# Performance work log

Measured on AMD Instinct MI355X. Metric: run time of the kernel, lower is better.

The kernel has to match this reference:

```python
import jax, jax.numpy as jnp
import numpy as np
import math

EMB = 64
NEG_INF = -1e30

def _layernorm(x, g, b, eps=1e-5):
    mu = jnp.mean(x, axis=-1, keepdims=True)
    var = jnp.mean((x - mu) ** 2, axis=-1, keepdims=True)
    return (x - mu) * jax.lax.rsqrt(var + eps) * g + b

def setup_inputs() -> dict:
    key = jax.random.key(0)
    ks = jax.random.split(key, 8)
    b, t, n, d = 16, 12, 307, EMB
    s = 1.0 / math.sqrt(d)
    inp = {
        'x': jax.random.normal(ks[0], (b, t, n, d), dtype=jnp.float32),
        'stg': jax.random.uniform(ks[1], (b, n, t, n), dtype=jnp.float32),
        'topk': 3,
        'q_w': jax.random.normal(ks[2], (d, d), dtype=jnp.float32) * s,
        'q_b': jnp.zeros((d,), jnp.float32),
        'k_w': jax.random.normal(ks[3], (d, d), dtype=jnp.float32) * s,
        'k_b': jnp.zeros((d,), jnp.float32),
        'ln_g': jnp.ones((d,), jnp.float32),
        'ln_b': jnp.zeros((d,), jnp.float32),
        'ffn_ln_g': jnp.ones((d,), jnp.float32),
        'ffn_ln_b': jnp.zeros((d,), jnp.float32),
        'fc1_w': jax.random.normal(ks[4], (4 * d, d), dtype=jnp.float32) * s,
        'fc1_b': jnp.zeros((4 * d,), jnp.float32),
        'fc2_w': jax.random.normal(ks[5], (d, 4 * d), dtype=jnp.float32) * (0.5 * s),
        'fc2_b': jnp.zeros((d,), jnp.float32),
    }
    return inp

def reference(x, stg, topk, q_w, q_b, k_w, k_b, ln_g, ln_b, ffn_ln_g, ffn_ln_b, fc1_w, fc1_b, fc2_w, fc2_b):
    b, t, n, d = x.shape
    scale = 1.0 / math.sqrt(d)
    x_ = _layernorm(x, ln_g, ln_b)           # [b,t,n,d]
    y_ = x_[:, -1]                            # [b,n,d] last timestep
    q = y_ @ q_w.T + q_b                      # [b,n,d]
    k = x_ @ k_w.T + k_b                      # [b,t,n,d]
    dg = jnp.einsum('bnd,btmd->bntm', q, k) * scale
    sag = jax.nn.sigmoid(dg) * stg * scale    # gated scores [b,n,t,n]
    sag = sag.reshape(b, n, t * n)
    if topk > 0:
        kk = topk * n if topk < 5 else topk   # mirrors torch's self.topk *= n
        top_values, _ = jax.lax.top_k(sag, kk)
        thr = top_values[..., -1:]
        sag = jnp.where(sag > thr, sag, NEG_INF)  # strict >, as in torch code
    sag = jax.nn.softmax(sag, axis=-1).reshape(b, n, t, n)  # dropout in eval mode = identity
    o = jnp.einsum('bntm,btmd->bnd', sag, x_)
    h = o + y_
    # FFN: pre-norm residual MLP (LayerNorm -> Linear(d,4d) -> ReLU -> Linear(4d,d) + residual)
    z = _layernorm(h, ffn_ln_g, ffn_ln_b)
    z = jax.nn.relu(z @ fc1_w.T + fc1_b) @ fc2_w.T + fc2_b
    return h + z
```

## Files before the change

### kernel.cpp

```cpp
#include <hip/hip_runtime.h>

typedef __bf16 bf16x8 __attribute__((ext_vector_type(8)));
typedef float  f32x4  __attribute__((ext_vector_type(4)));
typedef unsigned short u16x8 __attribute__((ext_vector_type(8)));

constexpr int BB    = 16;
constexpr int TT    = 12;
constexpr int NN    = 307;
constexpr int TN    = TT * NN;
constexpr int ROWSX = BB * TT * NN;
constexpr int ROWSH = BB * NN;
constexpr int SST1  = 3712;
constexpr int SSTR  = 3840;
constexpr float SCALE = 0.125f;

__device__ __forceinline__ float wred_sum(float v) {
#pragma unroll
    for (int m = 32; m > 0; m >>= 1) v += __shfl_xor(v, m, 64);
    return v;
}

__global__ void fold_k(const float* __restrict__ qw, const float* __restrict__ qb,
                       const float* __restrict__ kw, const float* __restrict__ kb,
                       float* __restrict__ M, float* __restrict__ b2,
                       float* __restrict__ vv, float* __restrict__ cc) {
    int e = blockIdx.x, d = threadIdx.x;
    float acc = 0.f;
    for (int dp = 0; dp < 64; ++dp) acc += qw[dp * 64 + e] * kw[dp * 64 + d];
    M[e * 64 + d] = acc;
    float vp = wred_sum(qw[d * 64 + e] * kb[d]);
    if (d == 0) vv[e] = vp;
    if (e == 0) {
        float b = 0.f;
        for (int dp = 0; dp < 64; ++dp) b += qb[dp] * kw[dp * 64 + d];
        b2[d] = b;
        float cp = wred_sum(qb[d] * kb[d]);
        if (d == 0) *cc = cp;
    }
}

__global__ void wconv_k(const float* __restrict__ fc1w, const float* __restrict__ fc2w,
                        __bf16* __restrict__ fc1b16, __bf16* __restrict__ fc2b16) {
    int i = blockIdx.x * 256 + threadIdx.x;
    if (i < 16384) fc1b16[i] = (__bf16)fc1w[i];
    else fc2b16[i - 16384] = (__bf16)fc2w[i - 16384];
}

__global__ __launch_bounds__(256) void ln_k(const float* __restrict__ x,
                                            const float* __restrict__ g,
                                            const float* __restrict__ b,
                                            __bf16* __restrict__ xnb,
                                            float* __restrict__ y32) {
    int w = threadIdx.x >> 6, l = threadIdx.x & 63;
    int r = blockIdx.x * 4 + w;
    if (r >= ROWSX) return;
    float val = x[r * 64 + l];
    float mu  = wred_sum(val) * (1.f / 64.f);
    float dv  = val - mu;
    float var = wred_sum(dv * dv) * (1.f / 64.f);
    float xv  = dv * rsqrtf(var + 1e-5f) * g[l] + b[l];
    xnb[(size_t)r * 64 + l] = (__bf16)xv;
    int t = (r / NN) % TT;
    if (t == TT - 1) {
        int bbv = r / (NN * TT), n = r % NN;
        y32[(bbv * NN + n) * 64 + l] = xv;
    }
}

__global__ __launch_bounds__(256) void t_k(const __bf16* __restrict__ xnb,
                                           __bf16* __restrict__ xnT) {
    __shared__ unsigned short tile[64][65];
    int bb = blockIdx.y, j0 = blockIdx.x * 64, t = threadIdx.x;
    const unsigned short* src = (const unsigned short*)xnb;
    unsigned short* dst = (unsigned short*)xnT;
#pragma unroll
    for (int i = 0; i < 16; ++i) {
        int f = t + 256 * i, jr = f >> 6, dc = f & 63;
        int j = j0 + jr;
        tile[jr][dc] = (j < TN) ? src[((size_t)bb * TN + j) * 64 + dc] : (unsigned short)0;
    }
    __syncthreads();
#pragma unroll
    for (int i = 0; i < 16; ++i) {
        int f = t + 256 * i, d = f >> 6, jj = f & 63;
        dst[((size_t)bb * 64 + d) * SSTR + j0 + jj] = tile[jj][d];
    }
}

__global__ __launch_bounds__(256) void qt_k(const float* __restrict__ y32,
                                            const float* __restrict__ M,
                                            const float* __restrict__ b2,
                                            const float* __restrict__ vv,
                                            const float* __restrict__ ccp,
                                            __bf16* __restrict__ qtb,
                                            float* __restrict__ cq) {
    int w = threadIdx.x >> 6, l = threadIdx.x & 63;
    int rr = blockIdx.x * 4 + w;
    if (rr >= ROWSH) return;
    float y = y32[rr * 64 + l];
    float acc = b2[l];
#pragma unroll
    for (int e = 0; e < 64; ++e) acc += __shfl(y, e, 64) * M[e * 64 + l];
    qtb[(size_t)rr * 64 + l] = (__bf16)acc;
    float cp = wred_sum(y * vv[l]);
    if (l == 0) cq[rr] = cp + *ccp;
}

__global__ __launch_bounds__(256) void score_k(const __bf16* __restrict__ qtb,
                                               const float* __restrict__ cq,
                                               const __bf16* __restrict__ xnb,
                                               const float* __restrict__ stg,
                                               __bf16* __restrict__ sag) {
    __shared__ float sstg[64 * 132];
    int bb = blockIdx.z, n0 = blockIdx.y * 64, j0 = blockIdx.x * 128;
    int t = threadIdx.x;
    int w = t >> 6, lane = t & 63;
    int m16 = lane & 15, q4 = lane >> 4;

#pragma unroll
    for (int i = 0; i < 8; ++i) {
        int flat = t + i * 256;
        int row = flat >> 5, c4 = (flat & 31) * 4;
        int n = n0 + row;
        float4 v = {0.f, 0.f, 0.f, 0.f};
        if (n < NN) {
            size_t rb = (size_t)(bb * NN + n) * TN;
            int j = j0 + c4;
            if (j + 3 < TN) v = *(const float4*)(stg + rb + j);
            else {
                if (j + 0 < TN) v.x = stg[rb + j + 0];
                if (j + 1 < TN) v.y = stg[rb + j + 1];
                if (j + 2 < TN) v.z = stg[rb + j + 2];
                if (j + 3 < TN) v.w = stg[rb + j + 3];
            }
        }
        *(float4*)&sstg[row * 132 + c4] = v;
    }

    const bf16x8* ap = (const bf16x8*)(qtb + ((size_t)bb * NN + n0 + w * 16 + m16) * 64);
    bf16x8 a0 = ap[q4], a1 = ap[q4 + 4];
    f32x4 acc[8];
#pragma unroll
    for (int jt = 0; jt < 8; ++jt) {
        const bf16x8* bp = (const bf16x8*)(xnb + ((size_t)bb * TN + j0 + jt * 16 + m16) * 64);
        bf16x8 b0 = bp[q4], b1 = bp[q4 + 4];
        f32x4 c = {0.f, 0.f, 0.f, 0.f};
        c = __builtin_amdgcn_mfma_f32_16x16x32_bf16(a0, b0, c, 0, 0, 0);
        c = __builtin_amdgcn_mfma_f32_16x16x32_bf16(a1, b1, c, 0, 0, 0);
        acc[jt] = c;
    }
    int nbase = n0 + w * 16 + q4 * 4;
    float cn[4];
#pragma unroll
    for (int r = 0; r < 4; ++r) {
        int n = nbase + r;
        cn[r] = (n < NN) ? cq[bb * NN + n] : 0.f;
    }
    __syncthreads();

    u16x8 wvr[4];
#pragma unroll
    for (int r = 0; r < 4; ++r) {
        int nloc = w * 16 + q4 * 4 + r;
#pragma unroll
        for (int jt = 0; jt < 8; ++jt) {
            int j = j0 + jt * 16 + m16;
            float sv = sstg[nloc * 132 + jt * 16 + m16];
            float dg = (acc[jt][r] + cn[r]) * SCALE;
            float s  = 1.f / (1.f + __expf(-dg));
            float wv = (j < TN) ? s * sv * SCALE : 0.f;
            __bf16 wb16 = (__bf16)wv;
            wvr[r][jt] = *(unsigned short*)&wb16;
        }
    }
    __syncthreads();

    unsigned short* wb = (unsigned short*)sstg;
#pragma unroll
    for (int r = 0; r < 4; ++r) {
        int nloc = w * 16 + q4 * 4 + r;
#pragma unroll
        for (int jt = 0; jt < 8; ++jt)
            wb[nloc * 136 + jt * 16 + m16] = wvr[r][jt];
    }
    __syncthreads();

#pragma unroll
    for (int i = 0; i < 4; ++i) {
        int chunk = t + i * 256;
        int row = chunk >> 4, c8 = (chunk & 15) * 8;
        int n = n0 + row;
        if (n < NN) {
            u16x8 v = *(const u16x8*)&wb[row * 136 + c8];
            *(u16x8*)((unsigned short*)sag + (size_t)(bb * NN + n) * SST1 + j0 + c8) = v;
        }
    }
}

__global__ __launch_bounds__(256) void smax_k(__bf16* __restrict__ sagB,
                                              const int* __restrict__ topk_p) {
    int t = threadIdx.x;
    int wid = t >> 6, lane = t & 63;
    int row = blockIdx.x * 4 + wid;
    if (row >= ROWSH) return;

    int topkv = *topk_p;
    bool selAll = (topkv <= 0);
    int kk = 0;
    if (!selAll) {
        kk = (topkv < 5) ? topkv * NN : topkv;
        if (kk > TN) kk = TN;
    }

    u16x8* src = (u16x8*)((unsigned short*)sagB + (size_t)row * SST1);
    u16x8 va[8];
#pragma unroll
    for (int ci = 0; ci < 8; ++ci) {
        int c = lane + (ci << 6);
        u16x8 v = {0, 0, 0, 0, 0, 0, 0, 0};
        if (c < 464) v = src[c];
        va[ci] = v;
    }
    int vmb = 0;
#pragma unroll
    for (int ci = 0; ci < 8; ++ci)
#pragma unroll
        for (int e = 0; e < 8; ++e) vmb = max(vmb, (int)va[ci][e]);
#pragma unroll
    for (int m = 32; m > 0; m >>= 1) vmb = max(vmb, __shfl_xor(vmb, m, 64));
    float vmax = __uint_as_float(((unsigned)vmb) << 16);

    unsigned thrb = 0;
    if (!selAll) {
        unsigned lo = 0, hi = (unsigned)vmb;
        while (lo < hi) {
            unsigned mid = (lo + hi) >> 1;
            int cnt = 0;
#pragma unroll
            for (int ci = 0; ci < 8; ++ci)
#pragma unroll
                for (int e = 0; e < 8; ++e)
                    cnt += (int)__popcll(__ballot((unsigned)va[ci][e] > mid));
            if (cnt < kk) hi = mid; else lo = mid + 1;
        }
        thrb = lo;
    }

    float local = 0.f;
#pragma unroll
    for (int ci = 0; ci < 8; ++ci) {
        int c = lane + (ci << 6);
        int nvv = (c < 460) ? 8 : ((c == 460) ? 4 : 0);
#pragma unroll
        for (int e = 0; e < 8; ++e) {
            unsigned u = va[ci][e];
            bool sel = selAll ? (e < nvv) : (u > thrb);
            float ev = sel ? __expf(__uint_as_float(u << 16) - vmax) : 0.f;
            local += ev;
            __bf16 eb = (__bf16)ev;
            va[ci][e] = *(unsigned short*)&eb;
        }
    }
    local = wred_sum(local);
    bool uni = !(local > 0.f);
    float inv = uni ? 0.f : 1.f / local;
    float uval = 1.f / (float)TN;
#pragma unroll
    for (int ci = 0; ci < 8; ++ci) {
        int c = lane + (ci << 6);
        if (c < 464) {
            int nvv = (c < 460) ? 8 : ((c == 460) ? 4 : 0);
            bf16x8 o;
#pragma unroll
            for (int e = 0; e < 8; ++e) {
                if (uni) o[e] = (e < nvv) ? (__bf16)uval : (__bf16)0.f;
                else {
                    unsigned short us = va[ci][e];
                    float ev = (float)(*(__bf16*)&us);
                    o[e] = (__bf16)(ev * inv);
                }
            }
            *(bf16x8*)&src[c] = o;
        }
    }
}

__global__ __launch_bounds__(256) void pv_k(const __bf16* __restrict__ sagB,
                                            const __bf16* __restrict__ xnT,
                                            const float* __restrict__ y32,
                                            float* __restrict__ h) {
    int bb = blockIdx.y, n0 = blockIdx.x * 16;
    int wid = threadIdx.x >> 6, lane = threadIdx.x & 63;
    int m16 = lane & 15, q4 = lane >> 4;

    int arow = min(n0 + m16, NN - 1);
    const __bf16* ab  = sagB + (size_t)(bb * NN + arow) * SST1 + q4 * 8;
    const __bf16* bbp = xnT + ((size_t)bb * 64 + wid * 16 + m16) * SSTR + q4 * 8;

    f32x4 acc0 = {0.f, 0.f, 0.f, 0.f}, acc1 = {0.f, 0.f, 0.f, 0.f};
#pragma unroll 4
    for (int ks = 0; ks < 116; ks += 2) {
        bf16x8 a0 = *(const bf16x8*)(ab + ks * 32);
        bf16x8 b0 = *(const bf16x8*)(bbp + ks * 32);
        bf16x8 a1 = *(const bf16x8*)(ab + ks * 32 + 32);
        bf16x8 b1 = *(const bf16x8*)(bbp + ks * 32 + 32);
        acc0 = __builtin_amdgcn_mfma_f32_16x16x32_bf16(a0, b0, acc0, 0, 0, 0);
        acc1 = __builtin_amdgcn_mfma_f32_16x16x32_bf16(a1, b1, acc1, 0, 0, 0);
    }
#pragma unroll
    for (int r = 0; r < 4; ++r) {
        int n = n0 + q4 * 4 + r;
        if (n < NN) {
            size_t o = (size_t)(bb * NN + n) * 64 + wid * 16 + m16;
            h[o] = acc0[r] + acc1[r] + y32[o];
        }
    }
}

__global__ __launch_bounds__(256) void ffn_k(const float* __restrict__ h,
                                             const float* __restrict__ g,
                                             const float* __restrict__ bln,
                                             const __bf16* __restrict__ fc1b16,
                                             const float* __restrict__ fc1b,
                                             const __bf16* __restrict__ fc2b16,
                                             const float* __restrict__ fc2b,
                                             float* __restrict__ out) {
    __shared__ __bf16 zb[16 * 68];
    __shared__ __bf16 ab[16 * 264];
    int t = threadIdx.x, r0 = blockIdx.x * 16;
    int wid = t >> 6, lane = t & 63;
    int m16 = lane & 15, q4 = lane >> 4;

#pragma unroll
    for (int q = 0; q < 4; ++q) {
        int rl = wid * 4 + q;
        float val = h[(size_t)(r0 + rl) * 64 + lane];
        float mu  = wred_sum(val) * (1.f / 64.f);
        float dv  = val - mu;
        float var = wred_sum(dv * dv) * (1.f / 64.f);
        zb[rl * 68 + lane] = (__bf16)(dv * rsqrtf(var + 1e-5f) * g[lane] + bln[lane]);
    }
    __syncthreads();

    bf16x8 a0 = *(const bf16x8*)&zb[m16 * 68 + q4 * 8];
    bf16x8 a1 = *(const bf16x8*)&zb[m16 * 68 + 32 + q4 * 8];
#pragma unroll
    for (int jt2 = 0; jt2 < 4; ++jt2) {
        int j0t = (wid * 4 + jt2) * 16;
        const __bf16* bp = fc1b16 + (size_t)(j0t + m16) * 64 + q4 * 8;
        f32x4 c = {0.f, 0.f, 0.f, 0.f};
        c = __builtin_amdgcn_mfma_f32_16x16x32_bf16(a0, *(const bf16x8*)bp, c, 0, 0, 0);
        c = __builtin_amdgcn_mfma_f32_16x16x32_bf16(a1, *(const bf16x8*)(bp + 32), c, 0, 0, 0);
        int j = j0t + m16;
        float bias = fc1b[j];
#pragma unroll
        for (int r = 0; r < 4; ++r)
            ab[(q4 * 4 + r) * 264 + j] = (__bf16)fmaxf(c[r] + bias, 0.f);
    }
    __syncthreads();

    f32x4 c2a = {0.f, 0.f, 0.f, 0.f}, c2b = {0.f, 0.f, 0.f, 0.f};
    const __bf16* b2p = fc2b16 + (size_t)(wid * 16 + m16) * 256 + q4 * 8;
#pragma unroll
    for (int k8 = 0; k8 < 8; k8 += 2) {
        bf16x8 aa0 = *(const bf16x8*)&ab[m16 * 264 + k8 * 32 + q4 * 8];
        bf16x8 aa1 = *(const bf16x8*)&ab[m16 * 264 + (k8 + 1) * 32 + q4 * 8];
        c2a = __builtin_amdgcn_mfma_f32_16x16x32_bf16(aa0, *(const bf16x8*)(b2p + k8 * 32), c2a, 0, 0, 0);
        c2b = __builtin_amdgcn_mfma_f32_16x16x32_bf16(aa1, *(const bf16x8*)(b2p + (k8 + 1) * 32), c2b, 0, 0, 0);
    }
    int d = wid * 16 + m16;
    float bias2 = fc2b[d];
#pragma unroll
    for (int r = 0; r < 4; ++r) {
        size_t row = (size_t)(r0 + q4 * 4 + r);
        out[row * 64 + d] = h[row * 64 + d] + c2a[r] + c2b[r] + bias2;
    }
}

extern "C" void kernel_launch(void* const* d_in, const int* in_sizes, int n_in,
                              void* d_out, int out_size, void* d_ws, size_t ws_size,
                              hipStream_t stream) {
    const float* x    = (const float*)d_in[0];
    const float* stg  = (const float*)d_in[1];
    const int*   topk = (const int*)d_in[2];
    const float* qw   = (const float*)d_in[3];
    const float* qb   = (const float*)d_in[4];
    const float* kw   = (const float*)d_in[5];
    const float* kb   = (const float*)d_in[6];
    const float* lng  = (const float*)d_in[7];
    const float* lnb  = (const float*)d_in[8];
    const float* flng = (const float*)d_in[9];
    const float* flnb = (const float*)d_in[10];
    const float* fc1w = (const float*)d_in[11];
    const float* fc1b = (const float*)d_in[12];
    const float* fc2w = (const float*)d_in[13];
    const float* fc2b = (const float*)d_in[14];
    float* out = (float*)d_out;

    float* ws = (float*)d_ws;
    __bf16* xnb = (__bf16*)ws;
    float* p1   = ws + 1886208;
    __bf16* xnT = (__bf16*)p1;
    float* p2   = p1 + 1966080;
    __bf16* qtb = (__bf16*)p2;
    float* y32  = p2 + 157696;
    float* cq   = y32 + 314368;
    float* M    = cq + 4928;
    float* b2   = M + 4096;
    float* vv   = b2 + 64;
    float* cc   = vv + 64;
    __bf16* fc1b16 = (__bf16*)(cc + 16);
    __bf16* fc2b16 = (__bf16*)((float*)fc1b16 + 8192);
    __bf16* sag = (__bf16*)((float*)fc2b16 + 8192);
    float* h    = (float*)sag + 9116672;

    fold_k<<<64, 64, 0, stream>>>(qw, qb, kw, kb, M, b2, vv, cc);
    wconv_k<<<128, 256, 0, stream>>>(fc1w, fc2w, fc1b16, fc2b16);
    ln_k<<<(ROWSX + 3) / 4, 256, 0, stream>>>(x, lng, lnb, xnb, y32);
    t_k<<<dim3((TN + 63) / 64, BB), 256, 0, stream>>>(xnb, xnT);
    qt_k<<<(ROWSH + 3) / 4, 256, 0, stream>>>(y32, M, b2, vv, cc, qtb, cq);
    score_k<<<dim3((TN + 127) / 128, (NN + 63) / 64, BB), 256, 0, stream>>>(qtb, cq, xnb, stg, sag);
    smax_k<<<(ROWSH + 3) / 4, 256, 0, stream>>>(sag, topk);
    pv_k<<<dim3((NN + 15) / 16, BB), 256, 0, stream>>>(sag, xnT, y32, h);
    ffn_k<<<ROWSH / 16, 256, 0, stream>>>(h, flng, flnb, fc1b16, fc1b, fc2b16, fc2b, out);
}
```

Measured before the change: 292.4 us.

## Split PV reduction four ways, defer softmax normalization, read stg directly in score

The PV kernel now splits the 3712-long reduction into four K-chunks across a new grid dimension and writes partial sums that the FFN kernel adds together. Softmax no longer normalizes probabilities; it stores per-row sums that PV applies as a reciprocal scale, which removes one pass of bf16 rounding and multiplication. The score kernel drops its shared-memory staging of stg and loads the values straight from global memory with per-lane scalar reads. The split raises parallelism in PV at the cost of extra partial-sum traffic and reads in the FFN kernel. The direct stg loads may coalesce worse than the earlier float4 staging.

```diff
diff --git a/kernel.cpp b/kernel.cpp
--- a/kernel.cpp
+++ b/kernel.cpp
@@ -12,6 +12,8 @@
 constexpr int ROWSH = BB * NN;
 constexpr int SST1  = 3712;
 constexpr int SSTR  = 3840;
+constexpr int HPS   = ROWSH * 64;
+constexpr int KQ    = 928;
 constexpr float SCALE = 0.125f;
 
 __device__ __forceinline__ float wred_sum(float v) {
@@ -111,31 +113,11 @@
                                                const __bf16* __restrict__ xnb,
                                                const float* __restrict__ stg,
                                                __bf16* __restrict__ sag) {
-    __shared__ float sstg[64 * 132];
+    __shared__ unsigned short wb[64 * 136];
     int bb = blockIdx.z, n0 = blockIdx.y * 64, j0 = blockIdx.x * 128;
     int t = threadIdx.x;
     int w = t >> 6, lane = t & 63;
     int m16 = lane & 15, q4 = lane >> 4;
-
-#pragma unroll
-    for (int i = 0; i < 8; ++i) {
-        int flat = t + i * 256;
-        int row = flat >> 5, c4 = (flat & 31) * 4;
-        int n = n0 + row;
-        float4 v = {0.f, 0.f, 0.f, 0.f};
-        if (n < NN) {
-            size_t rb = (size_t)(bb * NN + n) * TN;
-            int j = j0 + c4;
-            if (j + 3 < TN) v = *(const float4*)(stg + rb + j);
-            else {
-                if (j + 0 < TN) v.x = stg[rb + j + 0];
-                if (j + 1 < TN) v.y = stg[rb + j + 1];
-                if (j + 2 < TN) v.z = stg[rb + j + 2];
-                if (j + 3 < TN) v.w = stg[rb + j + 3];
-            }
-        }
-        *(float4*)&sstg[row * 132 + c4] = v;
-    }
 
     const bf16x8* ap = (const bf16x8*)(qtb + ((size_t)bb * NN + n0 + w * 16 + m16) * 64);
     bf16x8 a0 = ap[q4], a1 = ap[q4 + 4];
@@ -156,32 +138,26 @@
         int n = nbase + r;
         cn[r] = (n < NN) ? cq[bb * NN + n] : 0.f;
     }
-    __syncthreads();
-
-    u16x8 wvr[4];
+
+    const float* stgb = stg + (size_t)bb * NN * TN;
 #pragma unroll
     for (int r = 0; r < 4; ++r) {
         int nloc = w * 16 + q4 * 4 + r;
+        const float* srow = stgb + (size_t)min(nbase + r, NN - 1) * TN;
+        u16x8 wvr;
 #pragma unroll
         for (int jt = 0; jt < 8; ++jt) {
             int j = j0 + jt * 16 + m16;
-            float sv = sstg[nloc * 132 + jt * 16 + m16];
+            float sv = (j < TN) ? srow[j] : 0.f;
             float dg = (acc[jt][r] + cn[r]) * SCALE;
             float s  = 1.f / (1.f + __expf(-dg));
             float wv = (j < TN) ? s * sv * SCALE : 0.f;
             __bf16 wb16 = (__bf16)wv;
-            wvr[r][jt] = *(unsigned short*)&wb16;
-        }
-    }
-    __syncthreads();
-
-    unsigned short* wb = (unsigned short*)sstg;
-#pragma unroll
-    for (int r = 0; r < 4; ++r) {
-        int nloc = w * 16 + q4 * 4 + r;
+            wvr[jt] = *(unsigned short*)&wb16;
+        }
 #pragma unroll
         for (int jt = 0; jt < 8; ++jt)
-            wb[nloc * 136 + jt * 16 + m16] = wvr[r][jt];
+            wb[nloc * 136 + jt * 16 + m16] = wvr[jt];
     }
     __syncthreads();
 
@@ -198,7 +174,8 @@
 }
 
 __global__ __launch_bounds__(256) void smax_k(__bf16* __restrict__ sagB,
-                                              const int* __restrict__ topk_p) {
+                                              const int* __restrict__ topk_p,
+                                              float* __restrict__ rsum) {
     int t = threadIdx.x;
     int wid = t >> 6, lane = t & 63;
     int row = blockIdx.x * 4 + wid;
@@ -263,24 +240,26 @@
     }
     local = wred_sum(local);
     bool uni = !(local > 0.f);
-    float inv = uni ? 0.f : 1.f / local;
-    float uval = 1.f / (float)TN;
-#pragma unroll
-    for (int ci = 0; ci < 8; ++ci) {
-        int c = lane + (ci << 6);
-        if (c < 464) {
-            int nvv = (c < 460) ? 8 : ((c == 460) ? 4 : 0);
-            bf16x8 o;
-#pragma unroll
-            for (int e = 0; e < 8; ++e) {
-                if (uni) o[e] = (e < nvv) ? (__bf16)uval : (__bf16)0.f;
-                else {
-                    unsigned short us = va[ci][e];
-                    float ev = (float)(*(__bf16*)&us);
-                    o[e] = (__bf16)(ev * inv);
-                }
+    if (lane == 0) rsum[row] = uni ? (float)TN : local;
+
+    if (uni) {
+        __bf16 one = (__bf16)1.f, zero = (__bf16)0.f;
+#pragma unroll
+        for (int ci = 0; ci < 8; ++ci) {
+            int c = lane + (ci << 6);
+            if (c < 464) {
+                int nvv = (c < 460) ? 8 : ((c == 460) ? 4 : 0);
+                bf16x8 o;
+#pragma unroll
+                for (int e = 0; e < 8; ++e) o[e] = (e < nvv) ? one : zero;
+                *(bf16x8*)&src[c] = o;
             }
-            *(bf16x8*)&src[c] = o;
+        }
+    } else {
+#pragma unroll
+        for (int ci = 0; ci < 8; ++ci) {
+            int c = lane + (ci << 6);
+            if (c < 464) src[c] = va[ci];
         }
     }
 }
@@ -288,36 +267,38 @@
 __global__ __launch_bounds__(256) void pv_k(const __bf16* __restrict__ sagB,
                                             const __bf16* __restrict__ xnT,
                                             const float* __restrict__ y32,
-                                            float* __restrict__ h) {
-    int bb = blockIdx.y, n0 = blockIdx.x * 16;
+                                            const float* __restrict__ rsum,
+                                            float* __restrict__ hp) {
+    int bb = blockIdx.z, kq = blockIdx.y, n0 = blockIdx.x * 16;
     int wid = threadIdx.x >> 6, lane = threadIdx.x & 63;
     int m16 = lane & 15, q4 = lane >> 4;
 
     int arow = min(n0 + m16, NN - 1);
-    const __bf16* ab  = sagB + (size_t)(bb * NN + arow) * SST1 + q4 * 8;
-    const __bf16* bbp = xnT + ((size_t)bb * 64 + wid * 16 + m16) * SSTR + q4 * 8;
+    const __bf16* ab  = sagB + (size_t)(bb * NN + arow) * SST1 + kq * KQ + q4 * 8;
+    const __bf16* bbp = xnT + ((size_t)bb * 64 + wid * 16 + m16) * SSTR + kq * KQ + q4 * 8;
 
     f32x4 acc0 = {0.f, 0.f, 0.f, 0.f}, acc1 = {0.f, 0.f, 0.f, 0.f};
 #pragma unroll 4
-    for (int ks = 0; ks < 116; ks += 2) {
-        bf16x8 a0 = *(const bf16x8*)(ab + ks * 32);
-        bf16x8 b0 = *(const bf16x8*)(bbp + ks * 32);
-        bf16x8 a1 = *(const bf16x8*)(ab + ks * 32 + 32);
-        bf16x8 b1 = *(const bf16x8*)(bbp + ks * 32 + 32);
-        acc0 = __builtin_amdgcn_mfma_f32_16x16x32_bf16(a0, b0, acc0, 0, 0, 0);
-        acc1 = __builtin_amdgcn_mfma_f32_16x16x32_bf16(a1, b1, acc1, 0, 0, 0);
+    for (int ks = 0; ks < 29; ++ks) {
+        bf16x8 a = *(const bf16x8*)(ab + ks * 32);
+        bf16x8 b = *(const bf16x8*)(bbp + ks * 32);
+        if (ks & 1) acc1 = __builtin_amdgcn_mfma_f32_16x16x32_bf16(a, b, acc1, 0, 0, 0);
+        else        acc0 = __builtin_amdgcn_mfma_f32_16x16x32_bf16(a, b, acc0, 0, 0, 0);
     }
 #pragma unroll
     for (int r = 0; r < 4; ++r) {
         int n = n0 + q4 * 4 + r;
         if (n < NN) {
             size_t o = (size_t)(bb * NN + n) * 64 + wid * 16 + m16;
-            h[o] = acc0[r] + acc1[r] + y32[o];
-        }
-    }
-}
-
-__global__ __launch_bounds__(256) void ffn_k(const float* __restrict__ h,
+            float inv = 1.f / rsum[bb * NN + n];
+            float v = (acc0[r] + acc1[r]) * inv;
+            if (kq == 0) v += y32[o];
+            hp[(size_t)kq * HPS + o] = v;
+        }
+    }
+}
+
+__global__ __launch_bounds__(256) void ffn_k(const float* __restrict__ hp,
                                              const float* __restrict__ g,
                                              const float* __restrict__ bln,
                                              const __bf16* __restrict__ fc1b16,
@@ -334,7 +315,8 @@
 #pragma unroll
     for (int q = 0; q < 4; ++q) {
         int rl = wid * 4 + q;
-        float val = h[(size_t)(r0 + rl) * 64 + lane];
+        size_t i = (size_t)(r0 + rl) * 64 + lane;
+        float val = hp[i] + hp[HPS + i] + hp[2 * HPS + i] + hp[3 * HPS + i];
         float mu  = wred_sum(val) * (1.f / 64.f);
         float dv  = val - mu;
         float var = wred_sum(dv * dv) * (1.f / 64.f);
@@ -373,7 +355,9 @@
 #pragma unroll
     for (int r = 0; r < 4; ++r) {
         size_t row = (size_t)(r0 + q4 * 4 + r);
-        out[row * 64 + d] = h[row * 64 + d] + c2a[r] + c2b[r] + bias2;
+        size_t o = row * 64 + d;
+        float hsum = hp[o] + hp[HPS + o] + hp[2 * HPS + o] + hp[3 * HPS + o];
+        out[o] = hsum + c2a[r] + c2b[r] + bias2;
     }
 }
 
@@ -412,7 +396,8 @@
     __bf16* fc1b16 = (__bf16*)(cc + 16);
     __bf16* fc2b16 = (__bf16*)((float*)fc1b16 + 8192);
     __bf16* sag = (__bf16*)((float*)fc2b16 + 8192);
-    float* h    = (float*)sag + 9116672;
+    float* hp   = (float*)sag + 9116672;
+    float* rsum = hp + 4 * HPS;
 
     fold_k<<<64, 64, 0, stream>>>(qw, qb, kw, kb, M, b2, vv, cc);
     wconv_k<<<128, 256, 0, stream>>>(fc1w, fc2w, fc1b16, fc2b16);
@@ -420,7 +405,7 @@
     t_k<<<dim3((TN + 63) / 64, BB), 256, 0, stream>>>(xnb, xnT);
     qt_k<<<(ROWSH + 3) / 4, 256, 0, stream>>>(y32, M, b2, vv, cc, qtb, cq);
     score_k<<<dim3((TN + 127) / 128, (NN + 63) / 64, BB), 256, 0, stream>>>(qtb, cq, xnb, stg, sag);
-    smax_k<<<(ROWSH + 3) / 4, 256, 0, stream>>>(sag, topk);
-    pv_k<<<dim3((NN + 15) / 16, BB), 256, 0, stream>>>(sag, xnT, y32, h);
-    ffn_k<<<ROWSH / 16, 256, 0, stream>>>(h, flng, flnb, fc1b16, fc1b, fc2b16, fc2b, out);
-}
+    smax_k<<<(ROWSH + 3) / 4, 256, 0, stream>>>(sag, topk, rsum);
+    pv_k<<<dim3((NN + 15) / 16, 4, BB), 256, 0, stream>>>(sag, xnT, y32, rsum, hp);
+    ffn_k<<<ROWSH / 16, 256, 0, stream>>>(hp, flng, flnb, fc1b16, fc1b, fc2b16, fc2b, out);
+}
```

New measurement: 269.0 us. 8.0% less time.
